# Optimization experiments

Measured on AMD Instinct MI355X. Metric: run time of the kernel, lower is better.

The kernel has to match this reference:

```python
import math
import jax, jax.numpy as jnp
import numpy as np

NUM_HEADS = 16

def setup_inputs() -> dict:
    key = jax.random.key(0)
    ks = jax.random.split(key, 6)
    B, S, d = 16, 1024, 1024
    scale = 1.0 / math.sqrt(d)
    x = jax.random.normal(ks[0], (B, S, d), dtype=jnp.float32)
    Wq = jax.random.normal(ks[1], (d, d), dtype=jnp.float32) * scale
    Wk = jax.random.normal(ks[2], (d, d), dtype=jnp.float32) * scale
    Wv = jax.random.normal(ks[3], (d, d), dtype=jnp.float32) * scale
    Wo = jax.random.normal(ks[4], (d, d), dtype=jnp.float32) * scale
    z = jnp.zeros((d,), dtype=jnp.float32)
    return {"x": x, "Wq": Wq, "bq": z, "Wk": Wk, "bk": z, "Wv": Wv, "bv": z, "Wo": Wo, "bo": z}

def _split_heads(t, H):
    B, S, d = t.shape
    return t.reshape(B, S, H, d // H).transpose(0, 2, 1, 3)  # [B,H,S,dh]

def reference(x, Wq, bq, Wk, bk, Wv, bv, Wo, bo):
    B, S, d = x.shape
    H = NUM_HEADS
    dh = d // H
    # torch Linear: x @ W.T + b
    Q = _split_heads(x @ Wq.T + bq, H)
    K = _split_heads(x @ Wk.T + bk, H)
    V = _split_heads(x @ Wv.T + bv, H)
    scores = jnp.einsum('bhqd,bhkd->bhqk', Q, K)  # [B,H,S,S]
    causal = jnp.arange(S)[None, :] <= jnp.arange(S)[:, None]  # [S,S] True = allowed
    mask = (1.0 - causal.astype(jnp.float32)) * -100000.0
    # NOTE: original divides (scores + mask) by sqrt(dh), mask included
    attn = jax.nn.softmax((scores + mask) / math.sqrt(dh), axis=-1)
    out = jnp.einsum('bhqk,bhkd->bhqd', attn, V)  # [B,H,S,dh]
    out = out.transpose(0, 2, 1, 3).reshape(B, S, d)
    return out @ Wo.T + bo
```

## Files before the change

kernel.cpp:

```cpp
#include <hip/hip_runtime.h>

#define B_  16
#define S_  1024
#define D_  1024
#define H_  16
#define DH_ 64
#define M_  (B_ * S_)
#define BH_ (B_ * H_)

typedef __attribute__((ext_vector_type(8))) __bf16 bf16x8;
typedef __attribute__((ext_vector_type(4))) float  f32x4;

__device__ __forceinline__ ushort f2bf(float f) {
  unsigned u = __builtin_bit_cast(unsigned, f);
  return (ushort)((u + 0x7FFFu + ((u >> 16) & 1u)) >> 16);
}

__device__ __forceinline__ bf16x8 ld8(const ushort* p) {
  return *(const bf16x8*)p;
}

__device__ __forceinline__ float fast_exp2(float x) {
  return __builtin_amdgcn_exp2f(x);
}

__device__ __forceinline__ void gl_lds16(const void* g, void* s) {
  __builtin_amdgcn_global_load_lds((__attribute__((address_space(1))) void*)g,
                                   (__attribute__((address_space(3))) void*)s,
                                   16, 0, 0);
}

__global__ void cvt4(const float* __restrict__ s, ushort* __restrict__ d, int n4) {
  int i = blockIdx.x * 256 + threadIdx.x;
  if (i < n4) {
    const float4 v = ((const float4*)s)[i];
    ushort4 o;
    o.x = f2bf(v.x); o.y = f2bf(v.y); o.z = f2bf(v.z); o.w = f2bf(v.w);
    ((ushort4*)d)[i] = o;
  }
}

__global__ void gemm_qkv(const ushort* __restrict__ A, const ushort* __restrict__ Wqkv,
                         const float* __restrict__ bqp, const float* __restrict__ bkp,
                         const float* __restrict__ bvp, ushort* __restrict__ qO,
                         ushort* __restrict__ kO, ushort* __restrict__ vtO) {
  __shared__ ushort lA[128 * 32];
  __shared__ ushort lB[128 * 32];
  const int w  = threadIdx.x >> 6;
  const int l  = threadIdx.x & 63;
  const int m0 = blockIdx.y * 128, n0 = blockIdx.x * 128;
  const int srow = (w << 4) + (l >> 2);
  const int scol = (l & 3) << 3;
  const int lr = l & 15, qd = l >> 4;
  const int wm = (w >> 1) << 6, wn = (w & 1) << 6;
  const int K = D_;

  const f32x4 z = {0.f, 0.f, 0.f, 0.f};
  f32x4 acc[4][4];
#pragma unroll
  for (int i = 0; i < 4; i++)
#pragma unroll
    for (int j = 0; j < 4; j++) acc[i][j] = z;

  for (int k0 = 0; k0 < K; k0 += 32) {
#pragma unroll
    for (int r = 0; r < 2; r++) {
      const int row = r * 64 + srow;
      gl_lds16(A    + (size_t)(m0 + row) * K + k0 + scol, &lA[row * 32 + scol]);
      gl_lds16(Wqkv + (size_t)(n0 + row) * K + k0 + scol, &lB[row * 32 + scol]);
    }
    __syncthreads();
    bf16x8 af[4], bf_[4];
#pragma unroll
    for (int t = 0; t < 4; t++) {
      af[t]  = ld8(&lA[(wm + t * 16 + lr) * 32 + qd * 8]);
      bf_[t] = ld8(&lB[(wn + t * 16 + lr) * 32 + qd * 8]);
    }
#pragma unroll
    for (int i = 0; i < 4; i++)
#pragma unroll
      for (int j = 0; j < 4; j++)
        acc[i][j] = __builtin_amdgcn_mfma_f32_16x16x32_bf16(af[i], bf_[j], acc[i][j], 0, 0, 0);
    __syncthreads();
  }

  const int proj = n0 >> 10;
  const float* bias = (proj == 0) ? bqp : (proj == 1) ? bkp : bvp;
  ushort* outH = (proj == 0) ? qO : (proj == 1) ? kO : vtO;
  const int nb = n0 & 1023;

#pragma unroll
  for (int j = 0; j < 4; j++) {
    const int n = nb + wn + j * 16 + lr;
    const float bv = bias[n];
    const int h = n >> 6, dc = n & 63;
#pragma unroll
    for (int i = 0; i < 4; i++) {
      const f32x4 v = acc[i][j];
#pragma unroll
      for (int r = 0; r < 4; r++) {
        const int m = m0 + wm + i * 16 + qd * 4 + r;
        const int b = m >> 10, s = m & 1023;
        const float val = v[r] + bv;
        if (proj < 2)
          outH[((size_t)(b * H_ + h) * S_ + s) * DH_ + dc] = f2bf(val);
        else
          outH[((size_t)(b * H_ + h) * DH_ + dc) * S_ + s] = f2bf(val);
      }
    }
  }
}

__global__ void gemm_out(const ushort* __restrict__ A, const ushort* __restrict__ W,
                         const float* __restrict__ bias, float* __restrict__ outF) {
  __shared__ ushort lA[128 * 32];
  __shared__ ushort lB[128 * 32];
  const int w  = threadIdx.x >> 6;
  const int l  = threadIdx.x & 63;
  const int m0 = blockIdx.y * 128, n0 = blockIdx.x * 128;
  const int srow = (w << 4) + (l >> 2);
  const int scol = (l & 3) << 3;
  const int lr = l & 15, qd = l >> 4;
  const int wm = (w >> 1) << 6, wn = (w & 1) << 6;
  const int K = D_, N = D_;

  const f32x4 z = {0.f, 0.f, 0.f, 0.f};
  f32x4 acc[4][4];
#pragma unroll
  for (int i = 0; i < 4; i++)
#pragma unroll
    for (int j = 0; j < 4; j++) acc[i][j] = z;

  for (int k0 = 0; k0 < K; k0 += 32) {
#pragma unroll
    for (int r = 0; r < 2; r++) {
      const int row = r * 64 + srow;
      gl_lds16(A + (size_t)(m0 + row) * K + k0 + scol, &lA[row * 32 + scol]);
      gl_lds16(W + (size_t)(n0 + row) * K + k0 + scol, &lB[row * 32 + scol]);
    }
    __syncthreads();
    bf16x8 af[4], bf_[4];
#pragma unroll
    for (int t = 0; t < 4; t++) {
      af[t]  = ld8(&lA[(wm + t * 16 + lr) * 32 + qd * 8]);
      bf_[t] = ld8(&lB[(wn + t * 16 + lr) * 32 + qd * 8]);
    }
#pragma unroll
    for (int i = 0; i < 4; i++)
#pragma unroll
      for (int j = 0; j < 4; j++)
        acc[i][j] = __builtin_amdgcn_mfma_f32_16x16x32_bf16(af[i], bf_[j], acc[i][j], 0, 0, 0);
    __syncthreads();
  }

#pragma unroll
  for (int j = 0; j < 4; j++) {
    const int n = n0 + wn + j * 16 + lr;
    const float bv = bias[n];
#pragma unroll
    for (int i = 0; i < 4; i++) {
      const f32x4 v = acc[i][j];
#pragma unroll
      for (int r = 0; r < 4; r++) {
        const int m = m0 + wm + i * 16 + qd * 4 + r;
        outF[(size_t)m * N + n] = v[r] + bv;
      }
    }
  }
}

#define PSTR 40
__global__ __launch_bounds__(256) void attn_kernel(
    const ushort* __restrict__ Q, const ushort* __restrict__ K,
    const ushort* __restrict__ Vt, ushort* __restrict__ O) {
  __shared__ ushort lP[4][64 * PSTR];
  const int bh = blockIdx.y;
  const int w = threadIdx.x >> 6, l = threadIdx.x & 63;
  const int lr = l & 15, qd = l >> 4;
  const int p = blockIdx.x * 4 + w;
  const size_t base = (size_t)bh * (S_ * DH_);
  const ushort* Qb = Q + base;
  const ushort* Kb = K + base;
  const ushort* Vb = Vt + (size_t)bh * (DH_ * S_);
  ushort* myP = &lP[w][0];
  const int b = bh >> 4, h = bh & 15;
  const float C = 0.18033688011112042f;
  const f32x4 z = {0.f, 0.f, 0.f, 0.f};

#pragma unroll 1
  for (int tt = 0; tt < 2; tt++) {
    const int q0 = (tt == 0 ? p : 15 - p) * 64;

    bf16x8 bq[4][2];
#pragma unroll
    for (int qt = 0; qt < 4; qt++)
#pragma unroll
      for (int kc = 0; kc < 2; kc++)
        bq[qt][kc] = ld8(Qb + (size_t)(q0 + qt * 16 + lr) * DH_ + kc * 32 + qd * 8);

    f32x4 acc[4][4];
#pragma unroll
    for (int i = 0; i < 4; i++)
#pragma unroll
      for (int j = 0; j < 4; j++) acc[i][j] = z;
    float li[4] = {0.f, 0.f, 0.f, 0.f};

    for (int kb = 0; kb < q0 + 64; kb += 32) {
      bf16x8 ak[2][2];
#pragma unroll
      for (int kt = 0; kt < 2; kt++)
#pragma unroll
        for (int kc = 0; kc < 2; kc++)
          ak[kt][kc] = ld8(Kb + (size_t)(kb + kt * 16 + lr) * DH_ + kc * 32 + qd * 8);
      bf16x8 av[4];
#pragma unroll
      for (int dt = 0; dt < 4; dt++)
        av[dt] = ld8(Vb + (size_t)(dt * 16 + lr) * S_ + kb + qd * 8);

      const bool diag = (kb + 31 >= q0);
#pragma unroll
      for (int kt = 0; kt < 2; kt++) {
        const int keyb = kb + kt * 16 + qd * 4;
#pragma unroll
        for (int qt = 0; qt < 4; qt++) {
          f32x4 s = z;
          s = __builtin_amdgcn_mfma_f32_16x16x32_bf16(ak[kt][0], bq[qt][0], s, 0, 0, 0);
          s = __builtin_amdgcn_mfma_f32_16x16x32_bf16(ak[kt][1], bq[qt][1], s, 0, 0, 0);
          const int qq = q0 + qt * 16 + lr;
          float e0 = s[0] * C, e1 = s[1] * C, e2 = s[2] * C, e3 = s[3] * C;
          if (diag) {
            e0 = (keyb + 0 <= qq) ? e0 : -1e30f;
            e1 = (keyb + 1 <= qq) ? e1 : -1e30f;
            e2 = (keyb + 2 <= qq) ? e2 : -1e30f;
            e3 = (keyb + 3 <= qq) ? e3 : -1e30f;
          }
          const float p0 = fast_exp2(e0), p1 = fast_exp2(e1);
          const float p2 = fast_exp2(e2), p3 = fast_exp2(e3);
          li[qt] += (p0 + p1) + (p2 + p3);
          const uint d0 = __builtin_amdgcn_perm(__builtin_bit_cast(uint, p1),
                                                __builtin_bit_cast(uint, p0), 0x07060302u);
          const uint d1 = __builtin_amdgcn_perm(__builtin_bit_cast(uint, p3),
                                                __builtin_bit_cast(uint, p2), 0x07060302u);
          uint2 pk; pk.x = d0; pk.y = d1;
          *(uint2*)(myP + (qt * 16 + lr) * PSTR + kt * 16 + qd * 4) = pk;
        }
      }
#pragma unroll
      for (int qt = 0; qt < 4; qt++) {
        const bf16x8 bp = ld8(myP + (qt * 16 + lr) * PSTR + qd * 8);
#pragma unroll
        for (int dt = 0; dt < 4; dt++)
          acc[dt][qt] = __builtin_amdgcn_mfma_f32_16x16x32_bf16(av[dt], bp, acc[dt][qt], 0, 0, 0);
      }
    }

#pragma unroll
    for (int qt = 0; qt < 4; qt++) {
      float s = li[qt];
      s += __shfl_xor(s, 16);
      s += __shfl_xor(s, 32);
      const float inv = 1.f / s;
      const int q = q0 + qt * 16 + lr;
      ushort* orow = O + ((size_t)(b * S_ + q) * D_) + h * DH_ + qd * 4;
#pragma unroll
      for (int dt = 0; dt < 4; dt++) {
        const f32x4 v = acc[dt][qt];
        uint2 pk;
        pk.x = (uint)f2bf(v[0] * inv) | ((uint)f2bf(v[1] * inv) << 16);
        pk.y = (uint)f2bf(v[2] * inv) | ((uint)f2bf(v[3] * inv) << 16);
        *(uint2*)(orow + dt * 16) = pk;
      }
    }
  }
}

extern "C" void kernel_launch(void* const* d_in, const int* in_sizes, int n_in,
                              void* d_out, int out_size, void* d_ws, size_t ws_size,
                              hipStream_t stream) {
  const float* x  = (const float*)d_in[0];
  const float* Wq = (const float*)d_in[1];
  const float* bq = (const float*)d_in[2];
  const float* Wk = (const float*)d_in[3];
  const float* bk = (const float*)d_in[4];
  const float* Wv = (const float*)d_in[5];
  const float* bv = (const float*)d_in[6];
  const float* Wo = (const float*)d_in[7];
  const float* bo = (const float*)d_in[8];
  float* out = (float*)d_out;

  char* ws = (char*)d_ws;
  ushort* xb   = (ushort*)(ws);
  ushort* qb   = (ushort*)(ws + 33554432);
  ushort* kb   = (ushort*)(ws + 67108864);
  ushort* vtb  = (ushort*)(ws + 100663296);
  ushort* attn = (ushort*)(ws + 134217728);
  ushort* wqb  = (ushort*)(ws + 167772160);
  ushort* wkb  = (ushort*)(ws + 169869312);
  ushort* wvb  = (ushort*)(ws + 171966464);
  ushort* wob  = (ushort*)(ws + 174063616);

  cvt4<<<16384, 256, 0, stream>>>(x,  xb,  4194304);
  cvt4<<<1024,  256, 0, stream>>>(Wq, wqb, 262144);
  cvt4<<<1024,  256, 0, stream>>>(Wk, wkb, 262144);
  cvt4<<<1024,  256, 0, stream>>>(Wv, wvb, 262144);
  cvt4<<<1024,  256, 0, stream>>>(Wo, wob, 262144);

  gemm_qkv<<<dim3(24, 128), 256, 0, stream>>>(xb, wqb, bq, bk, bv, qb, kb, vtb);

  attn_kernel<<<dim3(2, BH_), 256, 0, stream>>>(qb, kb, vtb, attn);

  gemm_out<<<dim3(8, 128), 256, 0, stream>>>(attn, wob, bo, out);
}
```

Baseline: 426.3 us.

## Halve attention query tile, vectorize GEMM epilogues, merge weight conversions

The attention kernel now gives each wave 32 queries instead of 64 and launches twice as many blocks, so more blocks are in flight and register pressure drops. In the Q/K and output GEMMs the MFMA operands are swapped so each lane holds four consecutive columns. That allows packed uint2 bf16 stores and float4 fp32 stores in place of scalar ones. The four weight conversion launches are merged into one kernel. The trade-off is that each key/value tile loaded in attention is reused across fewer queries, which adds K/V load traffic.

```diff
diff --git a/kernel.cpp b/kernel.cpp
--- a/kernel.cpp
+++ b/kernel.cpp
@@ -30,6 +30,10 @@
                                    16, 0, 0);
 }
 
+__device__ __forceinline__ uint pack2(float a, float b) {
+  return (uint)f2bf(a) | ((uint)f2bf(b) << 16);
+}
+
 __global__ void cvt4(const float* __restrict__ s, ushort* __restrict__ d, int n4) {
   int i = blockIdx.x * 256 + threadIdx.x;
   if (i < n4) {
@@ -38,6 +42,18 @@
     o.x = f2bf(v.x); o.y = f2bf(v.y); o.z = f2bf(v.z); o.w = f2bf(v.w);
     ((ushort4*)d)[i] = o;
   }
+}
+
+__global__ void cvtW(const float* __restrict__ s0, const float* __restrict__ s1,
+                     const float* __restrict__ s2, const float* __restrict__ s3,
+                     ushort* __restrict__ d) {
+  int i = blockIdx.x * 256 + threadIdx.x;
+  const int j = i >> 18;
+  const float* s = (j == 0) ? s0 : (j == 1) ? s1 : (j == 2) ? s2 : s3;
+  const float4 v = ((const float4*)s)[i & 262143];
+  ushort4 o;
+  o.x = f2bf(v.x); o.y = f2bf(v.y); o.z = f2bf(v.z); o.w = f2bf(v.w);
+  ((ushort4*)d)[i] = o;
 }
 
 __global__ void gemm_qkv(const ushort* __restrict__ A, const ushort* __restrict__ Wqkv,
@@ -54,6 +70,8 @@
   const int lr = l & 15, qd = l >> 4;
   const int wm = (w >> 1) << 6, wn = (w & 1) << 6;
   const int K = D_;
+  const int proj = n0 >> 10;
+  const bool swp = (proj < 2);
 
   const f32x4 z = {0.f, 0.f, 0.f, 0.f};
   f32x4 acc[4][4];
@@ -76,36 +94,57 @@
       af[t]  = ld8(&lA[(wm + t * 16 + lr) * 32 + qd * 8]);
       bf_[t] = ld8(&lB[(wn + t * 16 + lr) * 32 + qd * 8]);
     }
-#pragma unroll
-    for (int i = 0; i < 4; i++)
-#pragma unroll
-      for (int j = 0; j < 4; j++)
-        acc[i][j] = __builtin_amdgcn_mfma_f32_16x16x32_bf16(af[i], bf_[j], acc[i][j], 0, 0, 0);
+    if (swp) {
+#pragma unroll
+      for (int i = 0; i < 4; i++)
+#pragma unroll
+        for (int j = 0; j < 4; j++)
+          acc[i][j] = __builtin_amdgcn_mfma_f32_16x16x32_bf16(bf_[j], af[i], acc[i][j], 0, 0, 0);
+    } else {
+#pragma unroll
+      for (int i = 0; i < 4; i++)
+#pragma unroll
+        for (int j = 0; j < 4; j++)
+          acc[i][j] = __builtin_amdgcn_mfma_f32_16x16x32_bf16(af[i], bf_[j], acc[i][j], 0, 0, 0);
+    }
     __syncthreads();
   }
 
-  const int proj = n0 >> 10;
-  const float* bias = (proj == 0) ? bqp : (proj == 1) ? bkp : bvp;
-  ushort* outH = (proj == 0) ? qO : (proj == 1) ? kO : vtO;
   const int nb = n0 & 1023;
-
-#pragma unroll
-  for (int j = 0; j < 4; j++) {
-    const int n = nb + wn + j * 16 + lr;
-    const float bv = bias[n];
-    const int h = n >> 6, dc = n & 63;
-#pragma unroll
-    for (int i = 0; i < 4; i++) {
-      const f32x4 v = acc[i][j];
-#pragma unroll
-      for (int r = 0; r < 4; r++) {
-        const int m = m0 + wm + i * 16 + qd * 4 + r;
+  if (swp) {
+    const float* bias = (proj == 0) ? bqp : bkp;
+    ushort* outH = (proj == 0) ? qO : kO;
+#pragma unroll
+    for (int j = 0; j < 4; j++) {
+      const int n = nb + wn + j * 16 + qd * 4;
+      const float4 b4 = *(const float4*)(bias + n);
+      const int h = n >> 6, dc = n & 63;
+#pragma unroll
+      for (int i = 0; i < 4; i++) {
+        const int m = m0 + wm + i * 16 + lr;
         const int b = m >> 10, s = m & 1023;
-        const float val = v[r] + bv;
-        if (proj < 2)
-          outH[((size_t)(b * H_ + h) * S_ + s) * DH_ + dc] = f2bf(val);
-        else
-          outH[((size_t)(b * H_ + h) * DH_ + dc) * S_ + s] = f2bf(val);
+        const f32x4 v = acc[i][j];
+        uint2 pk;
+        pk.x = pack2(v[0] + b4.x, v[1] + b4.y);
+        pk.y = pack2(v[2] + b4.z, v[3] + b4.w);
+        *(uint2*)(outH + ((size_t)(b * H_ + h) * S_ + s) * DH_ + dc) = pk;
+      }
+    }
+  } else {
+#pragma unroll
+    for (int j = 0; j < 4; j++) {
+      const int n = nb + wn + j * 16 + lr;
+      const float bv = bvp[n];
+      const int h = n >> 6, dc = n & 63;
+#pragma unroll
+      for (int i = 0; i < 4; i++) {
+        const int mb = m0 + wm + i * 16 + qd * 4;
+        const int b = mb >> 10, s = mb & 1023;
+        const f32x4 v = acc[i][j];
+        uint2 pk;
+        pk.x = pack2(v[0] + bv, v[1] + bv);
+        pk.y = pack2(v[2] + bv, v[3] + bv);
+        *(uint2*)(vtO + ((size_t)(b * H_ + h) * DH_ + dc) * S_ + s) = pk;
       }
     }
   }
@@ -149,22 +188,22 @@
     for (int i = 0; i < 4; i++)
 #pragma unroll
       for (int j = 0; j < 4; j++)
-        acc[i][j] = __builtin_amdgcn_mfma_f32_16x16x32_bf16(af[i], bf_[j], acc[i][j], 0, 0, 0);
+        acc[i][j] = __builtin_amdgcn_mfma_f32_16x16x32_bf16(bf_[j], af[i], acc[i][j], 0, 0, 0);
     __syncthreads();
   }
 
 #pragma unroll
   for (int j = 0; j < 4; j++) {
-    const int n = n0 + wn + j * 16 + lr;
-    const float bv = bias[n];
+    const int n = n0 + wn + j * 16 + qd * 4;
+    const float4 b4 = *(const float4*)(bias + n);
 #pragma unroll
     for (int i = 0; i < 4; i++) {
+      const int m = m0 + wm + i * 16 + lr;
       const f32x4 v = acc[i][j];
-#pragma unroll
-      for (int r = 0; r < 4; r++) {
-        const int m = m0 + wm + i * 16 + qd * 4 + r;
-        outF[(size_t)m * N + n] = v[r] + bv;
-      }
+      float4 st;
+      st.x = v[0] + b4.x; st.y = v[1] + b4.y;
+      st.z = v[2] + b4.z; st.w = v[3] + b4.w;
+      *(float4*)(outF + (size_t)m * N + n) = st;
     }
   }
 }
@@ -173,7 +212,7 @@
 __global__ __launch_bounds__(256) void attn_kernel(
     const ushort* __restrict__ Q, const ushort* __restrict__ K,
     const ushort* __restrict__ Vt, ushort* __restrict__ O) {
-  __shared__ ushort lP[4][64 * PSTR];
+  __shared__ ushort lP[4][32 * PSTR];
   const int bh = blockIdx.y;
   const int w = threadIdx.x >> 6, l = threadIdx.x & 63;
   const int lr = l & 15, qd = l >> 4;
@@ -189,23 +228,23 @@
 
 #pragma unroll 1
   for (int tt = 0; tt < 2; tt++) {
-    const int q0 = (tt == 0 ? p : 15 - p) * 64;
-
-    bf16x8 bq[4][2];
-#pragma unroll
-    for (int qt = 0; qt < 4; qt++)
+    const int q0 = (tt == 0 ? p : 31 - p) * 32;
+
+    bf16x8 bq[2][2];
+#pragma unroll
+    for (int qt = 0; qt < 2; qt++)
 #pragma unroll
       for (int kc = 0; kc < 2; kc++)
         bq[qt][kc] = ld8(Qb + (size_t)(q0 + qt * 16 + lr) * DH_ + kc * 32 + qd * 8);
 
-    f32x4 acc[4][4];
+    f32x4 acc[4][2];
 #pragma unroll
     for (int i = 0; i < 4; i++)
 #pragma unroll
-      for (int j = 0; j < 4; j++) acc[i][j] = z;
-    float li[4] = {0.f, 0.f, 0.f, 0.f};
-
-    for (int kb = 0; kb < q0 + 64; kb += 32) {
+      for (int j = 0; j < 2; j++) acc[i][j] = z;
+    float li[2] = {0.f, 0.f};
+
+    for (int kb = 0; kb < q0 + 32; kb += 32) {
       bf16x8 ak[2][2];
 #pragma unroll
       for (int kt = 0; kt < 2; kt++)
@@ -222,7 +261,7 @@
       for (int kt = 0; kt < 2; kt++) {
         const int keyb = kb + kt * 16 + qd * 4;
 #pragma unroll
-        for (int qt = 0; qt < 4; qt++) {
+        for (int qt = 0; qt < 2; qt++) {
           f32x4 s = z;
           s = __builtin_amdgcn_mfma_f32_16x16x32_bf16(ak[kt][0], bq[qt][0], s, 0, 0, 0);
           s = __builtin_amdgcn_mfma_f32_16x16x32_bf16(ak[kt][1], bq[qt][1], s, 0, 0, 0);
@@ -246,7 +285,7 @@
         }
       }
 #pragma unroll
-      for (int qt = 0; qt < 4; qt++) {
+      for (int qt = 0; qt < 2; qt++) {
         const bf16x8 bp = ld8(myP + (qt * 16 + lr) * PSTR + qd * 8);
 #pragma unroll
         for (int dt = 0; dt < 4; dt++)
@@ -255,7 +294,7 @@
     }
 
 #pragma unroll
-    for (int qt = 0; qt < 4; qt++) {
+    for (int qt = 0; qt < 2; qt++) {
       float s = li[qt];
       s += __shfl_xor(s, 16);
       s += __shfl_xor(s, 32);
@@ -266,8 +305,8 @@
       for (int dt = 0; dt < 4; dt++) {
         const f32x4 v = acc[dt][qt];
         uint2 pk;
-        pk.x = (uint)f2bf(v[0] * inv) | ((uint)f2bf(v[1] * inv) << 16);
-        pk.y = (uint)f2bf(v[2] * inv) | ((uint)f2bf(v[3] * inv) << 16);
+        pk.x = pack2(v[0] * inv, v[1] * inv);
+        pk.y = pack2(v[2] * inv, v[3] * inv);
         *(uint2*)(orow + dt * 16) = pk;
       }
     }
@@ -295,19 +334,14 @@
   ushort* vtb  = (ushort*)(ws + 100663296);
   ushort* attn = (ushort*)(ws + 134217728);
   ushort* wqb  = (ushort*)(ws + 167772160);
-  ushort* wkb  = (ushort*)(ws + 169869312);
-  ushort* wvb  = (ushort*)(ws + 171966464);
   ushort* wob  = (ushort*)(ws + 174063616);
 
-  cvt4<<<16384, 256, 0, stream>>>(x,  xb,  4194304);
-  cvt4<<<1024,  256, 0, stream>>>(Wq, wqb, 262144);
-  cvt4<<<1024,  256, 0, stream>>>(Wk, wkb, 262144);
-  cvt4<<<1024,  256, 0, stream>>>(Wv, wvb, 262144);
-  cvt4<<<1024,  256, 0, stream>>>(Wo, wob, 262144);
+  cvt4<<<16384, 256, 0, stream>>>(x, xb, 4194304);
+  cvtW<<<4096, 256, 0, stream>>>(Wq, Wk, Wv, Wo, wqb);
 
   gemm_qkv<<<dim3(24, 128), 256, 0, stream>>>(xb, wqb, bq, bk, bv, qb, kb, vtb);
 
-  attn_kernel<<<dim3(2, BH_), 256, 0, stream>>>(qb, kb, vtb, attn);
+  attn_kernel<<<dim3(4, BH_), 256, 0, stream>>>(qb, kb, vtb, attn);
 
   gemm_out<<<dim3(8, 128), 256, 0, stream>>>(attn, wob, bo, out);
 }
```

Measured after the change: 1.544 ms. 3.62x slower.
